# Optimization experiments

Measured on AMD Instinct MI355X. Metric: run time of the kernel, lower is better.

The kernel has to match this reference:

```python
import jax, jax.numpy as jnp
import numpy as np

INPUT_SCALE = 1.0
RES_SCALE = 0.9


def setup_inputs() -> dict:
    key = jax.random.key(0)
    k1, k2, k3, k4 = jax.random.split(key, 4)
    seq_len, input_size, res_size = 4096, 128, 2048
    return {
        "input_data": jax.random.normal(k1, (seq_len, input_size), dtype=jnp.float32),
        "initial_state": jax.random.normal(k2, (res_size,), dtype=jnp.float32),
        "W_in": jax.random.normal(k3, (res_size, input_size), dtype=jnp.float32),
        "W_res": jax.random.normal(k4, (res_size, res_size), dtype=jnp.float32),
    }


def reference(input_data, initial_state, W_in, W_res):
    # input_data: (seq_len, input_size); returns states: (seq_len+1, res_size)
    res_size = W_res.shape[0]
    inv_sqrt_n = 1.0 / np.sqrt(res_size).astype(np.float32)
    # Precompute input projections for all timesteps in one GEMM: (seq_len, res)
    u_proj = INPUT_SCALE * (input_data @ W_in.T)

    def step(state, u_t):
        new_state = jnp.tanh(u_t + RES_SCALE * (W_res @ state)) * inv_sqrt_n
        return new_state, new_state

    _, states_tail = jax.lax.scan(step, initial_state, u_proj)
    return jnp.concatenate([initial_state[None, :], states_tail], axis=0)
```

## Files before the change

kernel.cpp:

```cpp
#include <hip/hip_runtime.h>
#include <hip/hip_fp16.h>
#include <stdint.h>


#define RES     2048
#define ROWSPW  4
#define WPB     16
#define ROWSPB  (ROWSPW * WPB)
#define NBLK    (RES / ROWSPB)
#define NUNITS  (RES / 2)
#define UPB     (ROWSPB / 2)
#define PPL     16

typedef _Float16 half2v __attribute__((ext_vector_type(2)));

union H2U { half2v h; uint32_t u; };

__device__ __forceinline__ uint32_t pack_h2(float a, float b) {
  H2U c; c.h.x = (_Float16)a; c.h.y = (_Float16)b; return c.u;
}
__device__ __forceinline__ half2v u_to_h2(uint32_t u) { H2U c; c.u = u; return c.h; }

__device__ __forceinline__ float dot2acc(uint32_t wu, uint32_t su, float acc) {
#if __has_builtin(__builtin_amdgcn_fdot2)
  return __builtin_amdgcn_fdot2(u_to_h2(wu), u_to_h2(su), acc, false);
#else
  half2v w = u_to_h2(wu), s = u_to_h2(su);
  acc = fmaf((float)w.x, (float)s.x, acc);
  return fmaf((float)w.y, (float)s.y, acc);
#endif
}

__device__ __forceinline__ float fast_tanh(float x) {
  float e = __expf(2.0f * x);
  return 1.0f - 2.0f / (e + 1.0f);
}

__device__ __forceinline__ float merge_red(float lo, float hi, int mask, int lane) {
  float sel  = (lane & mask) ? lo : hi;
  float keep = (lane & mask) ? hi : lo;
  return keep + __shfl_xor(sel, mask);
}

__global__ void reservoir_init(const float* __restrict__ s0,
                               float* __restrict__ out,
                               uint64_t* __restrict__ buf0,
                               uint64_t* __restrict__ buf1,
                               int res) {
  int i = blockIdx.x * blockDim.x + threadIdx.x;
  if (i < res) out[i] = s0[i];
  if (i < res / 2) {
    uint32_t a = (uint32_t)__half_as_ushort(__float2half_rn(s0[2 * i]));
    uint32_t b = (uint32_t)__half_as_ushort(__float2half_rn(s0[2 * i + 1]));
    buf0[i] = (uint64_t)(a | (b << 16));
    buf1[i] = 0xFFFFFFFF00000000ull;
  }
}

__global__ void __launch_bounds__(1024, 4)
reservoir_main(const float* __restrict__ in,
               const float* __restrict__ W_in,
               const float* __restrict__ W_res,
               float* __restrict__ out,
               uint64_t* __restrict__ buf0,
               uint64_t* __restrict__ buf1,
               int seq, int isz) {
  const int lane = threadIdx.x & 63;
  const int q    = threadIdx.x >> 6;
  const int W    = blockIdx.x * WPB + q;
  const int r0   = W * ROWSPW;

  __shared__ uint32_t pay[2][NUNITS];
  __shared__ uint32_t ous[UPB];

  uint32_t w[ROWSPW][PPL];
#pragma unroll
  for (int r = 0; r < ROWSPW; ++r) {
    const float* wr = W_res + (size_t)(r0 + r) * RES;
#pragma unroll
    for (int j = 0; j < PPL; ++j) {
      float2 p2 = *(const float2*)(wr + 2 * (lane + 64 * j));
      w[r][j] = pack_h2(0.9f * p2.x, 0.9f * p2.y);
    }
  }
#pragma unroll
  for (int r = 0; r < ROWSPW; ++r)
#pragma unroll
    for (int j = 0; j < PPL; ++j)
      asm("" : "+v"(w[r][j]));

  float win[ROWSPW][2];
#pragma unroll
  for (int r = 0; r < ROWSPW; ++r) {
    float2 p2 = *(const float2*)(W_in + (size_t)(r0 + r) * isz + 2 * lane);
    win[r][0] = p2.x;
    win[r][1] = p2.y;
  }

  const float inv_sqrt_n = 0.022097086912079612f;

  float2 xin = *(const float2*)(in + 2 * lane);

  const int upos = q * 64 + lane;

  for (int t = 0; t < seq; ++t) {
    const int p = t & 1;
    const uint64_t* src = p ? buf1 : buf0;
    uint64_t* dst       = p ? buf0 : buf1;
    const uint32_t want = (uint32_t)t;

    uint32_t dw;
    for (;;) {
      uint64_t v = __hip_atomic_load(src + upos, __ATOMIC_RELAXED,
                                     __HIP_MEMORY_SCOPE_AGENT);
      if (__all((uint32_t)(v >> 32) == want)) { dw = (uint32_t)v; break; }
    }

    pay[p][upos] = dw;
    __syncthreads();

    float acc[ROWSPW];
#pragma unroll
    for (int r = 0; r < ROWSPW; ++r)
      acc[r] = fmaf(xin.y, win[r][1], xin.x * win[r][0]);

#pragma unroll
    for (int j = 0; j < PPL; ++j) {
      uint32_t sv = pay[p][lane + 64 * j];
#pragma unroll
      for (int r = 0; r < ROWSPW; ++r)
        acc[r] = dot2acc(w[r][j], sv, acc[r]);
    }

    float m0 = merge_red(acc[0], acc[1], 1, lane);
    float m1 = merge_red(acc[2], acc[3], 1, lane);
    float qq = merge_red(m0, m1, 2, lane);
    qq += __shfl_xor(qq, 4);
    qq += __shfl_xor(qq, 8);
    qq += __shfl_xor(qq, 16);
    qq += __shfl_xor(qq, 32);

    float o = fast_tanh(qq) * inv_sqrt_n;

    uint32_t hu = (uint32_t)__half_as_ushort(__float2half_rn(o));
    uint32_t up = (uint32_t)__shfl_xor((int)hu, 1);
    uint32_t word = (hu & 0xffffu) | (up << 16);
    if (lane == 0 || lane == 2)
      ous[2 * q + (lane >> 1)] = word;

    if (lane < ROWSPW)
      out[(size_t)(t + 1) * RES + r0 + lane] = o;

    __syncthreads();

    if (q == 0 && lane < UPB) {
      uint64_t val = ((uint64_t)(uint32_t)(t + 1) << 32) | (uint64_t)ous[lane];
      __hip_atomic_store(dst + UPB * blockIdx.x + lane, val, __ATOMIC_RELAXED,
                         __HIP_MEMORY_SCOPE_AGENT);
    }

    int tn = (t + 1 < seq) ? (t + 1) : t;
    xin = *(const float2*)(in + (size_t)tn * isz + 2 * lane);
  }
}

extern "C" void kernel_launch(void* const* d_in, const int* in_sizes, int n_in,
                              void* d_out, int out_size, void* d_ws, size_t ws_size,
                              hipStream_t stream) {
  const float* input = (const float*)d_in[0];
  const float* s0    = (const float*)d_in[1];
  const float* W_in  = (const float*)d_in[2];
  const float* W_res = (const float*)d_in[3];
  float* out = (float*)d_out;

  const int res = in_sizes[1];
  const int isz = in_sizes[2] / res;
  const int seq = in_sizes[0] / isz;

  uint64_t* buf0 = (uint64_t*)d_ws;
  uint64_t* buf1 = buf0 + res / 2;

  reservoir_init<<<(res + 255) / 256, 256, 0, stream>>>(s0, out, buf0, buf1, res);
  reservoir_main<<<NBLK, WPB * 64, 0, stream>>>(input, W_in, W_res, out,
                                                buf0, buf1, seq, isz);
}
```

Measured before the change: 7.991 ms.

## Halve warps per block and publish state directly per warp, dropping second barrier

Each block now holds 8 waves instead of 16, doubling the block count to 64. Each wave polls two flag-tagged words from the shared state buffer. Every wave now publishes its own output words straight to global memory with tagged atomic stores, which removes the staging through shared memory and the second block-wide barrier on each timestep. The intent is a shorter critical path in the per-step cross-block handoff. The cost is more blocks participating in the grid-wide spin synchronisation and more global polling traffic per wave.

```diff
diff --git a/kernel.cpp b/kernel.cpp
--- a/kernel.cpp
+++ b/kernel.cpp
@@ -5,11 +5,11 @@
 
 #define RES     2048
 #define ROWSPW  4
-#define WPB     16
+#define WPB     8
 #define ROWSPB  (ROWSPW * WPB)
 #define NBLK    (RES / ROWSPB)
 #define NUNITS  (RES / 2)
-#define UPB     (ROWSPB / 2)
+#define UPW     (NUNITS / WPB / 64)
 #define PPL     16
 
 typedef _Float16 half2v __attribute__((ext_vector_type(2)));
@@ -57,7 +57,7 @@
   }
 }
 
-__global__ void __launch_bounds__(1024, 4)
+__global__ void __launch_bounds__(512, 2)
 reservoir_main(const float* __restrict__ in,
                const float* __restrict__ W_in,
                const float* __restrict__ W_res,
@@ -71,7 +71,6 @@
   const int r0   = W * ROWSPW;
 
   __shared__ uint32_t pay[2][NUNITS];
-  __shared__ uint32_t ous[UPB];
 
   uint32_t w[ROWSPW][PPL];
 #pragma unroll
@@ -101,7 +100,7 @@
 
   float2 xin = *(const float2*)(in + 2 * lane);
 
-  const int upos = q * 64 + lane;
+  const int ubase = q * (NUNITS / WPB) + lane;
 
   for (int t = 0; t < seq; ++t) {
     const int p = t & 1;
@@ -109,14 +108,27 @@
     uint64_t* dst       = p ? buf0 : buf1;
     const uint32_t want = (uint32_t)t;
 
-    uint32_t dw;
+    uint32_t dw[UPW];
     for (;;) {
-      uint64_t v = __hip_atomic_load(src + upos, __ATOMIC_RELAXED,
-                                     __HIP_MEMORY_SCOPE_AGENT);
-      if (__all((uint32_t)(v >> 32) == want)) { dw = (uint32_t)v; break; }
+      uint64_t v[UPW];
+#pragma unroll
+      for (int k = 0; k < UPW; ++k)
+        v[k] = __hip_atomic_load(src + ubase + 64 * k, __ATOMIC_RELAXED,
+                                 __HIP_MEMORY_SCOPE_AGENT);
+      bool ok = true;
+#pragma unroll
+      for (int k = 0; k < UPW; ++k)
+        ok &= ((uint32_t)(v[k] >> 32) == want);
+      if (__all(ok)) {
+#pragma unroll
+        for (int k = 0; k < UPW; ++k) dw[k] = (uint32_t)v[k];
+        break;
+      }
     }
 
-    pay[p][upos] = dw;
+#pragma unroll
+    for (int k = 0; k < UPW; ++k)
+      pay[p][ubase + 64 * k] = dw[k];
     __syncthreads();
 
     float acc[ROWSPW];
@@ -145,20 +157,13 @@
     uint32_t hu = (uint32_t)__half_as_ushort(__float2half_rn(o));
     uint32_t up = (uint32_t)__shfl_xor((int)hu, 1);
     uint32_t word = (hu & 0xffffu) | (up << 16);
+    uint64_t val  = ((uint64_t)(uint32_t)(t + 1) << 32) | (uint64_t)word;
     if (lane == 0 || lane == 2)
-      ous[2 * q + (lane >> 1)] = word;
+      __hip_atomic_store(dst + 2 * W + (lane >> 1), val, __ATOMIC_RELAXED,
+                         __HIP_MEMORY_SCOPE_AGENT);
 
     if (lane < ROWSPW)
       out[(size_t)(t + 1) * RES + r0 + lane] = o;
-
-    __syncthreads();
-
-    if (q == 0 && lane < UPB) {
-      uint64_t val = ((uint64_t)(uint32_t)(t + 1) << 32) | (uint64_t)ous[lane];
-      __hip_atomic_store(dst + UPB * blockIdx.x + lane, val, __ATOMIC_RELAXED,
-                         __HIP_MEMORY_SCOPE_AGENT);
-    }
-
     int tn = (t + 1 < seq) ? (t + 1) : t;
     xin = *(const float2*)(in + (size_t)tn * isz + 2 * lane);
   }
```

New measurement: 8.973 ms. 12.3% more time.
